# Kernel tuning notes

Measured on AMD Instinct MI355X. Metric: run time of the kernel, lower is better.

The kernel has to match this reference:

```python
import jax, jax.numpy as jnp
import numpy as np

ROWS, COLS, CH, K = 8, 8, 32, 3
D = ROWS * COLS * CH  # state_dim = 2048


def _conv1d(x, w, b):
    # x: (N, C_in, L), w: (C_out, C_in, K) -- SAME padding = kernel//2 for odd K
    out = jax.lax.conv_general_dilated(x, w, window_strides=(1,), padding='SAME',
                                       dimension_numbers=('NCH', 'OIH', 'NCH'))
    return out + b[None, :, None]


def _cell(x, h, c, wx, bx, wh, bh):
    # RowSharedConvLSTMCell: x (B,ROWS,C_in,COLS), h/c (B,ROWS,CH,COLS)
    B = x.shape[0]
    xr = x.reshape(B * ROWS, x.shape[2], COLS)
    hr = h.reshape(B * ROWS, CH, COLS)
    gates = _conv1d(xr, wx, bx) + _conv1d(hr, wh, bh)
    i, f, o, g = jnp.split(gates, 4, axis=1)
    cr = jax.nn.sigmoid(f) * c.reshape(B * ROWS, CH, COLS) + jax.nn.sigmoid(i) * jnp.tanh(g)
    hr2 = jax.nn.sigmoid(o) * jnp.tanh(cr)
    return hr2.reshape(B, ROWS, CH, COLS), cr.reshape(B, ROWS, CH, COLS)


def _inter(state, enc, w, b):
    # scores h_d^T H_e -> softmax over encoder positions -> context -> tanh fuse
    scores = jnp.einsum('bsd,bd->bs', enc, state)
    a = jax.nn.softmax(scores, axis=1)
    ctx = jnp.einsum('bsd,bs->bd', enc, a)
    return jnp.tanh(jnp.concatenate([state, ctx], axis=-1) @ w + b)


def _self_step(state, pre_hist, ref_hist, t, w, b):
    # score against refined history, aggregate pre-self history; causal mask i < t
    T = pre_hist.shape[0]
    scores = jnp.einsum('tbd,bd->bt', ref_hist, state)
    mask = (jnp.arange(T) < t)[None, :]
    a = jax.nn.softmax(jnp.where(mask, scores, -1e9), axis=1)
    ctx = jnp.einsum('tbd,bt->bd', pre_hist, a) * (t > 0)  # zero context at step 0
    return jnp.tanh(jnp.concatenate([state, ctx], axis=-1) @ w + b)


def _forward(x_flat, encoder_outputs, h0, c0,
             cx_w0, cx_b0, ch_w0, ch_b0, cx_w1, cx_b1, ch_w1, ch_b1,
             ia_w0, ia_b0, sa_w0, sa_b0, ia_w1, ia_b1, sa_w1, sa_b1,
             hw1, hb1, hw2, hb2, hw3, hb3):
    B, T, _ = x_flat.shape
    xseq = x_flat.reshape(B, T, ROWS, COLS)[:, :, :, None, :]   # (B,T,ROWS,1,COLS)
    xseq = jnp.transpose(xseq, (1, 0, 2, 3, 4))                 # (T,B,ROWS,1,COLS)
    zhist = jnp.zeros((T, B, D), x_flat.dtype)
    carry = (h0[0], c0[0], h0[1], c0[1], zhist, zhist, zhist, zhist)

    def step(carry, xs):
        hA, cA, hB, cB, p0, r0, p1, r1 = carry
        xt, t = xs
        # layer 0: ConvLSTM -> inter-attn -> self-attn
        hraw0, cn0 = _cell(xt, hA, cA, cx_w0, cx_b0, ch_w0, ch_b0)
        hi0 = _inter(hraw0.reshape(B, D), encoder_outputs, ia_w0, ia_b0)
        hr0 = _self_step(hi0, p0, r0, t, sa_w0, sa_b0)
        p0 = p0.at[t].set(hi0)
        r0 = r0.at[t].set(hr0)
        # layer 1, fed with refined layer-0 output reshaped to frame
        hraw1, cn1 = _cell(hr0.reshape(B, ROWS, CH, COLS), hB, cB, cx_w1, cx_b1, ch_w1, ch_b1)
        hi1 = _inter(hraw1.reshape(B, D), encoder_outputs, ia_w1, ia_b1)
        hr1 = _self_step(hi1, p1, r1, t, sa_w1, sa_b1)
        p1 = p1.at[t].set(hi1)
        r1 = r1.at[t].set(hr1)
        # prediction head (eval-mode dropout = identity)
        z = jax.nn.relu(hr1 @ hw1 + hb1)
        z = jax.nn.relu(z @ hw2 + hb2)
        logits = z @ hw3 + hb3
        # hidden carries raw ConvLSTM h (matches original new_hidden.append((h_raw, c_new)))
        return (hraw0, cn0, hraw1, cn1, p0, r0, p1, r1), logits

    _, logits_seq = jax.lax.scan(step, carry, (xseq, jnp.arange(T)))
    return jnp.transpose(logits_seq, (1, 0, 2))  # (B, T, output_dim)


def setup_inputs() -> dict:
    key = jax.random.key(0)
    ks = jax.random.split(key, 16)
    B, T, S, OUT = 128, 64, 128, 2
    n = jax.random.normal
    f32 = jnp.float32
    inp = {
        'x_flat': n(ks[0], (B, T, ROWS * COLS), f32),
        'encoder_outputs': n(ks[1], (B, S, D), f32) * 0.05,
        'h0': jnp.zeros((2, B, ROWS, CH, COLS), f32),
        'c0': jnp.zeros((2, B, ROWS, CH, COLS), f32),
        'cx_w0': n(ks[2], (4 * CH, 1, K), f32) / float(np.sqrt(1 * K)),
        'cx_b0': jnp.zeros((4 * CH,), f32),
        'ch_w0': n(ks[3], (4 * CH, CH, K), f32) / float(np.sqrt(CH * K)),
        'ch_b0': jnp.zeros((4 * CH,), f32),
        'cx_w1': n(ks[4], (4 * CH, CH, K), f32) / float(np.sqrt(CH * K)),
        'cx_b1': jnp.zeros((4 * CH,), f32),
        'ch_w1': n(ks[5], (4 * CH, CH, K), f32) / float(np.sqrt(CH * K)),
        'ch_b1': jnp.zeros((4 * CH,), f32),
        'ia_w0': n(ks[6], (2 * D, D), f32) / float(np.sqrt(2 * D)),
        'ia_b0': jnp.zeros((D,), f32),
        'sa_w0': n(ks[7], (2 * D, D), f32) / float(np.sqrt(2 * D)),
        'sa_b0': jnp.zeros((D,), f32),
        'ia_w1': n(ks[8], (2 * D, D), f32) / float(np.sqrt(2 * D)),
        'ia_b1': jnp.zeros((D,), f32),
        'sa_w1': n(ks[9], (2 * D, D), f32) / float(np.sqrt(2 * D)),
        'sa_b1': jnp.zeros((D,), f32),
        'hw1': n(ks[10], (D, 200), f32) / float(np.sqrt(D)),
        'hb1': jnp.zeros((200,), f32),
        'hw2': n(ks[11], (200, 50), f32) / float(np.sqrt(200.0)),
        'hb2': jnp.zeros((50,), f32),
        'hw3': n(ks[12], (50, OUT), f32) / float(np.sqrt(50.0)),
        'hb3': jnp.zeros((OUT,), f32),
    }
    return inp


def reference(x_flat, encoder_outputs, h0, c0,
              cx_w0, cx_b0, ch_w0, ch_b0, cx_w1, cx_b1, ch_w1, ch_b1,
              ia_w0, ia_b0, sa_w0, sa_b0, ia_w1, ia_b1, sa_w1, sa_b1,
              hw1, hb1, hw2, hb2, hw3, hb3):
    return _forward(x_flat, encoder_outputs, h0, c0,
                    cx_w0, cx_b0, ch_w0, ch_b0, cx_w1, cx_b1, ch_w1, ch_b1,
                    ia_w0, ia_b0, sa_w0, sa_b0, ia_w1, ia_b1, sa_w1, sa_b1,
                    hw1, hb1, hw2, hb2, hw3, hb3)
```

## Files before the change

### kernel.cpp

```cpp
#include <hip/hip_runtime.h>
#include <math.h>


typedef _Float16 f16;
typedef _Float16 f16x8 __attribute__((ext_vector_type(8)));
typedef _Float16 f16x4 __attribute__((ext_vector_type(4)));
typedef _Float16 f16x2 __attribute__((ext_vector_type(2)));
typedef float  f32x16 __attribute__((ext_vector_type(16)));
typedef float  f32x4v __attribute__((ext_vector_type(4)));
typedef float  f32x2v __attribute__((ext_vector_type(2)));
typedef unsigned short u16x8 __attribute__((ext_vector_type(8)));
typedef unsigned short u16x4 __attribute__((ext_vector_type(4)));

#define BD 262144
#define XGT 1048576

__device__ __forceinline__ unsigned short f2bf(float x){
  unsigned int u = __builtin_bit_cast(unsigned int, x);
  u += 0x7fffu + ((u >> 16) & 1u);
  return (unsigned short)(u >> 16);
}
__device__ __forceinline__ float bf2f(unsigned short h){
  unsigned int u = ((unsigned int)h) << 16;
  return __builtin_bit_cast(float, u);
}
__device__ __forceinline__ float sigmoidf_(float x){
  return 1.0f / (1.0f + __expf(-x));
}
__device__ __forceinline__ void g2l16(const void* g, void* l){
  __builtin_amdgcn_global_load_lds(
      (const __attribute__((address_space(1))) unsigned int*)g,
      (__attribute__((address_space(3))) unsigned int*)l,
      16, 0, 0);
}

__global__ __launch_bounds__(256) void k_transpose_f16(
    const float* __restrict__ src, f16* __restrict__ dhi,
    const int K, const int N)
{
  __shared__ float tile[32][33];
  const int n0 = blockIdx.x * 32, k0 = blockIdx.y * 32;
  const int tx = threadIdx.x & 31, ty = threadIdx.x >> 5;
  #pragma unroll
  for (int ii = 0; ii < 4; ++ii){
    const int k = k0 + ty + ii*8, n = n0 + tx;
    float v = (n < N) ? src[(size_t)k * N + n] : 0.0f;
    tile[ty + ii*8][tx] = v;
  }
  __syncthreads();
  #pragma unroll
  for (int ii = 0; ii < 4; ++ii){
    const int n = n0 + ty + ii*8, k = k0 + tx;
    dhi[(size_t)n * K + k] = (f16)tile[tx][ty + ii*8];
  }
}

__global__ __launch_bounds__(256) void k_enc_prep(
    const float* __restrict__ enc,
    f16* __restrict__ encF, f16* __restrict__ encT)
{
  __shared__ float tile[32][33];
  const int dt = blockIdx.x;
  const int st = blockIdx.y;
  const int b  = blockIdx.z;
  const int tx = threadIdx.x & 31, ty = threadIdx.x >> 5;
  const int d0 = dt*32, s0 = st*32;
  #pragma unroll
  for (int ii = 0; ii < 4; ++ii){
    const int s = s0 + ty + ii*8, d = d0 + tx;
    const float v = enc[((size_t)b*128 + s)*2048 + d];
    tile[ty + ii*8][tx] = v;
    encF[((size_t)b*128 + s)*2048 + d] = (f16)v;
  }
  __syncthreads();
  #pragma unroll
  for (int ii = 0; ii < 4; ++ii){
    const int d = d0 + ty + ii*8, s = s0 + tx;
    encT[((size_t)b*2048 + d)*128 + s] = (f16)tile[tx][ty + ii*8];
  }
}

__global__ void k_pack_cellw(const float* __restrict__ chw,
                             const float* __restrict__ cxw,
                             unsigned short* __restrict__ wh16,
                             unsigned short* __restrict__ wcx16)
{
  const int i = blockIdx.x * 256 + threadIdx.x;
  if (i < 128 * 32){
    const int gc = i >> 5, icg = i & 31;
    #pragma unroll
    for (int k = 0; k < 3; ++k){
      wh16[(icg*3 + k)*128 + gc]  = f2bf(chw[i*3 + k]);
      wcx16[(icg*3 + k)*128 + gc] = f2bf(cxw[i*3 + k]);
    }
  }
}

__global__ __launch_bounds__(256) void k_cell0(
    const float* __restrict__ x_flat,
    const float* __restrict__ h0, const float* __restrict__ c0,
    const float* __restrict__ cxw, const float* __restrict__ cxb,
    const float* __restrict__ chw, const float* __restrict__ chb,
    f16* __restrict__ hrawHi)
{
  const int b = blockIdx.x >> 3, row = blockIdx.x & 7;
  const int tid = threadIdx.x;
  __shared__ float h_lds[264];
  __shared__ float x_lds[8];
  __shared__ float P[128][2][9];
  const int gc = tid >> 1, ih = tid & 1;
  float wh[16][3];
  #pragma unroll
  for (int icl = 0; icl < 16; ++icl)
    #pragma unroll
    for (int k = 0; k < 3; ++k)
      wh[icl][k] = chw[(gc*32 + ih*16 + icl)*3 + k];
  const float wx0 = cxw[gc*3+0], wx1 = cxw[gc*3+1], wx2 = cxw[gc*3+2];
  const float bsum = cxb[gc] + chb[gc];
  const int ic = tid >> 3, col = tid & 7;
  const size_t dg = (size_t)b*2048 + row*256 + tid;
  const int wofs = tid + ((tid >> 7) << 2);
  const int hbase = ih * 132;
  float c_reg = c0[dg];
  h_lds[wofs] = h0[dg];
  float xnext = (tid < 8) ? x_flat[((size_t)b*64 + 0)*64 + row*8 + tid] : 0.f;
  __syncthreads();
  for (int t = 0; t < 64; ++t){
    if (tid < 8) x_lds[tid] = xnext;
    __syncthreads();
    if (t < 63 && tid < 8)
      xnext = x_flat[((size_t)b*64 + t + 1)*64 + row*8 + tid];
    float g8[8];
    #pragma unroll
    for (int c2 = 0; c2 < 8; ++c2) g8[c2] = 0.f;
    #pragma unroll
    for (int icl = 0; icl < 16; ++icl){
      const float* hb = &h_lds[icl*8 + hbase];
      f32x4v hv0 = *reinterpret_cast<const f32x4v*>(hb);
      f32x4v hv1 = *reinterpret_cast<const f32x4v*>(hb + 4);
      const float hv[8] = {hv0[0],hv0[1],hv0[2],hv0[3],hv1[0],hv1[1],hv1[2],hv1[3]};
      #pragma unroll
      for (int c2 = 0; c2 < 8; ++c2){
        float s = hv[c2] * wh[icl][1];
        if (c2 > 0) s += hv[c2-1] * wh[icl][0];
        if (c2 < 7) s += hv[c2+1] * wh[icl][2];
        g8[c2] += s;
      }
    }
    if (ih == 0){
      #pragma unroll
      for (int c2 = 0; c2 < 8; ++c2){
        float s = x_lds[c2] * wx1 + bsum;
        if (c2 > 0) s += x_lds[c2-1] * wx0;
        if (c2 < 7) s += x_lds[c2+1] * wx2;
        g8[c2] += s;
      }
    }
    #pragma unroll
    for (int c2 = 0; c2 < 8; ++c2) P[gc][ih][c2] = g8[c2];
    __syncthreads();
    const float ipre = P[ic   ][0][col] + P[ic   ][1][col];
    const float fpre = P[ic+32][0][col] + P[ic+32][1][col];
    const float opre = P[ic+64][0][col] + P[ic+64][1][col];
    const float gpre = P[ic+96][0][col] + P[ic+96][1][col];
    const float cn = sigmoidf_(fpre)*c_reg + sigmoidf_(ipre)*tanhf(gpre);
    c_reg = cn;
    const float hn = sigmoidf_(opre)*tanhf(cn);
    hrawHi[((size_t)t*128 + b)*2048 + row*256 + tid] = (f16)hn;
    __syncthreads();
    h_lds[wofs] = hn;
  }
}

__global__ __launch_bounds__(256) void k_xconv(
    const f16* __restrict__ r0Hi, const f16* __restrict__ r0Lo,
    const unsigned short* __restrict__ wcx16,
    f16* __restrict__ xg)
{
  const int b = blockIdx.x >> 3, row = blockIdx.x & 7;
  const int tc = blockIdx.y;
  const int tid = threadIdx.x;
  const int gc = tid >> 1, half = tid & 1;
  __shared__ float xs[8][256];
  __shared__ unsigned short wl[96*128];
  for (int i = tid; i < 96*128; i += 256) wl[i] = wcx16[i];
  const size_t dg = (size_t)b*2048 + row*256 + tid;
  #pragma unroll
  for (int tt = 0; tt < 8; ++tt){
    const size_t tb = (size_t)(tc*8 + tt)*BD + dg;
    xs[tt][tid] = (float)r0Hi[tb] + (float)r0Lo[tb];
  }
  __syncthreads();
  const int c0 = half*4;
  float acc0[8], acc1[8], acc2[8], acc3[8];
  #pragma unroll
  for (int tt = 0; tt < 8; ++tt){ acc0[tt]=0.f; acc1[tt]=0.f; acc2[tt]=0.f; acc3[tt]=0.f; }
  for (int ic2 = 0; ic2 < 32; ++ic2){
    const unsigned short* wq = &wl[ic2*3*128 + gc];
    const float wx0 = bf2f(wq[0]), wx1 = bf2f(wq[128]), wx2 = bf2f(wq[256]);
    #pragma unroll
    for (int tt = 0; tt < 8; ++tt){
      const float* xr = &xs[tt][ic2*8];
      {
        const int c = c0 + 0;
        float s = xr[c]*wx1;
        if (c > 0) s += xr[c-1]*wx0;
        s += xr[c+1]*wx2;
        acc0[tt] += s;
      }
      {
        const int c = c0 + 1;
        acc1[tt] += xr[c]*wx1 + xr[c-1]*wx0 + xr[c+1]*wx2;
      }
      {
        const int c = c0 + 2;
        acc2[tt] += xr[c]*wx1 + xr[c-1]*wx0 + xr[c+1]*wx2;
      }
      {
        const int c = c0 + 3;
        float s = xr[c]*wx1 + xr[c-1]*wx0;
        if (c < 7) s += xr[c+1]*wx2;
        acc3[tt] += s;
      }
    }
  }
  const size_t xgbase = ((size_t)b*8 + row)*1024 + gc*8 + half*4;
  #pragma unroll
  for (int tt = 0; tt < 8; ++tt){
    f16x4 o;
    o[0] = (f16)acc0[tt]; o[1] = (f16)acc1[tt];
    o[2] = (f16)acc2[tt]; o[3] = (f16)acc3[tt];
    *reinterpret_cast<f16x4*>(xg + (size_t)(tc*8 + tt)*XGT + xgbase) = o;
  }
}

__global__ __launch_bounds__(256) void k_cell1_all(
    const f16* __restrict__ xg,
    const float* __restrict__ h0s, const float* __restrict__ c0s,
    const unsigned short* __restrict__ wh16,
    const float* __restrict__ cxb, const float* __restrict__ chb,
    f16* __restrict__ hrw1Hi)
{
  const int b = blockIdx.x >> 3, row = blockIdx.x & 7;
  const int tid = threadIdx.x;
  __shared__ float h_lds[264];
  __shared__ float P[128][2][9];
  __shared__ unsigned short wlds16[96*128];
  const int gc = tid >> 1, ih = tid & 1;
  for (int i = tid; i < 96*128; i += 256) wlds16[i] = wh16[i];
  const size_t dg = (size_t)b*2048 + row*256 + tid;
  const int ic = tid >> 3, col = tid & 7;
  const float bi = cxb[ic]    + chb[ic];
  const float bf = cxb[ic+32] + chb[ic+32];
  const float bo = cxb[ic+64] + chb[ic+64];
  const float bg = cxb[ic+96] + chb[ic+96];
  const int wofs = tid + ((tid >> 7) << 2);
  const int hbase = ih * 132;
  const size_t xgbase = ((size_t)b*8 + row)*1024 + gc*8;
  float c_reg = c0s[dg];
  h_lds[wofs] = h0s[dg];
  f16x8 xgv;
  if (ih == 0) xgv = *reinterpret_cast<const f16x8*>(xg + xgbase);
  __syncthreads();
  for (int t = 0; t < 64; ++t){
    f16x8 xgn;
    if (ih == 0 && t < 63)
      xgn = *reinterpret_cast<const f16x8*>(xg + (size_t)(t+1)*XGT + xgbase);
    {
      float g8[8];
      #pragma unroll
      for (int c2 = 0; c2 < 8; ++c2) g8[c2] = 0.f;
      #pragma unroll
      for (int icl = 0; icl < 16; ++icl){
        const int icg = ih*16 + icl;
        const float* hb = &h_lds[icl*8 + hbase];
        f32x4v hv0 = *reinterpret_cast<const f32x4v*>(hb);
        f32x4v hv1 = *reinterpret_cast<const f32x4v*>(hb + 4);
        const float hv[8] = {hv0[0],hv0[1],hv0[2],hv0[3],hv1[0],hv1[1],hv1[2],hv1[3]};
        const unsigned short* wq = &wlds16[icg*3*128 + gc];
        const float wh0 = bf2f(wq[0]);
        const float wh1 = bf2f(wq[128]);
        const float wh2 = bf2f(wq[256]);
        #pragma unroll
        for (int c2 = 0; c2 < 8; ++c2){
          float s = hv[c2]*wh1;
          if (c2 > 0) s += hv[c2-1]*wh0;
          if (c2 < 7) s += hv[c2+1]*wh2;
          g8[c2] += s;
        }
      }
      if (ih == 0){
        #pragma unroll
        for (int c2 = 0; c2 < 8; ++c2) g8[c2] += (float)xgv[c2];
      }
      #pragma unroll
      for (int c2 = 0; c2 < 8; ++c2) P[gc][ih][c2] = g8[c2];
    }
    __syncthreads();
    {
      const float ipre = P[ic   ][0][col] + P[ic   ][1][col] + bi;
      const float fpre = P[ic+32][0][col] + P[ic+32][1][col] + bf;
      const float opre = P[ic+64][0][col] + P[ic+64][1][col] + bo;
      const float gpre = P[ic+96][0][col] + P[ic+96][1][col] + bg;
      const float cn = sigmoidf_(fpre)*c_reg + sigmoidf_(ipre)*tanhf(gpre);
      c_reg = cn;
      const float hraw = sigmoidf_(opre)*tanhf(cn);
      hrw1Hi[(size_t)t*BD + dg] = (f16)hraw;
      __syncthreads();
      h_lds[wofs] = hraw;
      if (ih == 0) xgv = xgn;
    }
  }
}

__global__ __launch_bounds__(256) void k_attn(
    const f16* __restrict__ encF,
    const f16* __restrict__ encT,
    const f16* __restrict__ stHi,
    f16* __restrict__ ctxHi)
{
  const int b = blockIdx.x, th = blockIdx.y;
  const int tid = threadIdx.x, lane = tid & 63, wv = tid >> 6;
  __shared__ float S_lds[128][36];
  __shared__ float red[8][32];
  __shared__ float colv[32];
  __shared__ __align__(16) char aT[8192];
  const int kb = lane >> 5;
  {
    const int rA = wv*32 + (lane & 31);
    const int tcol = th*32 + (lane & 31);
    const f16* pA  = encF + ((size_t)b*128 + rA)*2048 + kb*8;
    const f16* pBH = stHi + ((size_t)tcol*128 + b)*2048 + kb*8;
    f32x16 acc;
    #pragma unroll
    for (int r = 0; r < 16; ++r) acc[r] = 0.f;
    #pragma unroll 4
    for (int s = 0; s < 128; ++s){
      f16x8 av = *reinterpret_cast<const f16x8*>(pA  + s*16);
      f16x8 bh = *reinterpret_cast<const f16x8*>(pBH + s*16);
      acc = __builtin_amdgcn_mfma_f32_32x32x16_f16(av, bh, acc, 0, 0, 0);
    }
    #pragma unroll
    for (int r = 0; r < 16; ++r){
      const int rr = 4*kb + (r & 3) + 8*(r >> 2);
      S_lds[wv*32 + rr][lane & 31] = acc[r];
    }
  }
  __syncthreads();
  {
    const int c = tid & 31, g = tid >> 5;
    float ev[16];
    float m = -INFINITY;
    #pragma unroll
    for (int i = 0; i < 16; ++i){ ev[i] = S_lds[g*16 + i][c]; m = fmaxf(m, ev[i]); }
    red[g][c] = m;
    __syncthreads();
    if (tid < 32){
      float M = red[0][tid];
      #pragma unroll
      for (int j = 1; j < 8; ++j) M = fmaxf(M, red[j][tid]);
      colv[tid] = M;
    }
    __syncthreads();
    const float M = colv[c];
    float sum = 0.f;
    #pragma unroll
    for (int i = 0; i < 16; ++i){ ev[i] = __expf(ev[i] - M); sum += ev[i]; }
    __syncthreads();
    red[g][c] = sum;
    __syncthreads();
    if (tid < 32){
      float L = red[0][tid];
      #pragma unroll
      for (int j = 1; j < 8; ++j) L += red[j][tid];
      colv[tid] = 1.f / L;
    }
    __syncthreads();
    const float inv = colv[c];
    f16x8 w0, w1;
    #pragma unroll
    for (int j = 0; j < 8; ++j){
      w0[j] = (f16)(ev[j] * inv);
      w1[j] = (f16)(ev[8 + j] * inv);
    }
    const int sw = (c & 15) << 4;
    *reinterpret_cast<f16x8*>(aT + c*256 + (((g*2    )*16) ^ sw)) = w0;
    *reinterpret_cast<f16x8*>(aT + c*256 + (((g*2 + 1)*16) ^ sw)) = w1;
  }
  __syncthreads();
  {
    const int arow = lane & 31;
    const int asw = (arow & 15) << 4;
    f16x8 afr[8];
    #pragma unroll
    for (int ks = 0; ks < 8; ++ks){
      const int chunk = 2*ks + kb;
      afr[ks] = *reinterpret_cast<const f16x8*>(aT + arow*256 + ((chunk*16) ^ asw));
    }
    for (int nt = wv; nt < 64; nt += 4){
      const int d = nt*32 + (lane & 31);
      const f16* pB = encT + ((size_t)b*2048 + d)*128 + kb*8;
      f32x16 acc;
      #pragma unroll
      for (int r = 0; r < 16; ++r) acc[r] = 0.f;
      #pragma unroll
      for (int ks = 0; ks < 8; ++ks){
        f16x8 bv = *reinterpret_cast<const f16x8*>(pB + ks*16);
        acc = __builtin_amdgcn_mfma_f32_32x32x16_f16(afr[ks], bv, acc, 0, 0, 0);
      }
      #pragma unroll
      for (int r = 0; r < 16; ++r){
        const int rr = 4*kb + (r & 3) + 8*(r >> 2);
        const size_t o = ((size_t)(th*32 + rr)*128 + b)*2048 + d;
        ctxHi[o] = (f16)acc[r];
      }
    }
  }
}

__global__ __launch_bounds__(256, 2) void k_gemm_full(
    const f16* __restrict__ a0, const f16* __restrict__ a1,
    const f16* __restrict__ wHp, const float* __restrict__ bias,
    f16* __restrict__ outHi, f16* __restrict__ outLo)
{
  const int nt = blockIdx.x, t = blockIdx.y;
  const size_t tb = (size_t)t * BD;
  const int tid = threadIdx.x;
  const int lane = tid & 63, wv = tid >> 6;
  __shared__ __align__(16) char lds[49152];
  const f16* wH = wHp + (size_t)(nt*64)*4096;

  auto stage = [&](int buf, int ki){
    char* lb = lds + buf*24576;
    const f16* aH = ((ki < 32) ? a0 : a1) + tb;
    const int ke = (ki & 31) * 64;
    #pragma unroll
    for (int i = 0; i < 4; ++i){
      const int c = i*256 + tid, row = c >> 3;
      const int srcb = ((c & 7)*16) ^ ((row & 7) << 4);
      g2l16((const char*)(aH + (size_t)row*2048 + ke) + srcb, lb + c*16);
    }
    #pragma unroll
    for (int i = 0; i < 2; ++i){
      const int c = i*256 + tid, row = c >> 3;
      const int srcb = ((c & 7)*16) ^ ((row & 7) << 4);
      g2l16((const char*)(wH + (size_t)row*4096 + ki*64) + srcb, lb + 16384 + c*16);
    }
  };

  f32x16 acc0, acc1;
  #pragma unroll
  for (int r = 0; r < 16; ++r){ acc0[r] = 0.f; acc1[r] = 0.f; }
  const int rA = wv*32 + (lane & 31);
  const int kb = lane >> 5;
  const int rB0 = lane & 31;
  const int aswz = (rA & 7) << 4;
  const int bswz = (rB0 & 7) << 4;

  stage(0, 0);
  __syncthreads();
  for (int ki = 0; ki < 64; ++ki){
    const int buf = ki & 1;
    if (ki < 63) stage(buf ^ 1, ki + 1);
    const char* lb = lds + buf*24576;
    #pragma unroll
    for (int s = 0; s < 4; ++s){
      const int cb = s*32 + kb*16;
      f16x8 ah  = *reinterpret_cast<const f16x8*>(lb + rA*128 + (cb ^ aswz));
      f16x8 b0h = *reinterpret_cast<const f16x8*>(lb + 16384 + rB0*128 + (cb ^ bswz));
      f16x8 b1h = *reinterpret_cast<const f16x8*>(lb + 16384 + 4096 + rB0*128 + (cb ^ bswz));
      acc0 = __builtin_amdgcn_mfma_f32_32x32x16_f16(ah, b0h, acc0, 0, 0, 0);
      acc1 = __builtin_amdgcn_mfma_f32_32x32x16_f16(ah, b1h, acc1, 0, 0, 0);
    }
    __syncthreads();
  }

  const int col0 = nt*64 + (lane & 31);
  const float b0 = bias[col0], b1 = bias[col0 + 32];
  const int rowBase = wv*32 + 4*kb;
  #pragma unroll
  for (int r = 0; r < 16; ++r){
    const int rr = rowBase + (r & 3) + 8*(r >> 2);
    const size_t o = tb + (size_t)rr*2048 + col0;
    const float p = tanhf(acc0[r] + b0);
    const float q = tanhf(acc1[r] + b1);
    const f16 ph = (f16)p, qh = (f16)q;
    outHi[o]      = ph;  outLo[o]      = (f16)(p - (float)ph);
    outHi[o + 32] = qh;  outLo[o + 32] = (f16)(q - (float)qh);
  }
}

__global__ __launch_bounds__(256, 2) void k_gemm_full2(
    const f16* __restrict__ aHi,
    const f16* __restrict__ wSp,
    float* __restrict__ Y, f16* __restrict__ G)
{
  const int nt = blockIdx.x, t = blockIdx.y;
  const size_t tb = (size_t)t * BD;
  const int tid = threadIdx.x;
  const int lane = tid & 63, wv = tid >> 6;
  __shared__ __align__(16) char lds[49152];
  const f16* wH = wSp + (size_t)(nt*64)*2048;
  const f16* aH = aHi + tb;

  auto stage = [&](int buf, int ki){
    char* lb = lds + buf*24576;
    const int ke = ki*64;
    #pragma unroll
    for (int i = 0; i < 4; ++i){
      const int c = i*256 + tid, row = c >> 3;
      const int srcb = ((c & 7)*16) ^ ((row & 7) << 4);
      g2l16((const char*)(aH + (size_t)row*2048 + ke) + srcb, lb + c*16);
    }
    #pragma unroll
    for (int i = 0; i < 2; ++i){
      const int c = i*256 + tid, row = c >> 3;
      const int srcb = ((c & 7)*16) ^ ((row & 7) << 4);
      g2l16((const char*)(wH + (size_t)row*2048 + ke) + srcb, lb + 16384 + c*16);
    }
  };

  f32x16 acc0, acc1;
  #pragma unroll
  for (int r = 0; r < 16; ++r){ acc0[r] = 0.f; acc1[r] = 0.f; }
  const int rA = wv*32 + (lane & 31);
  const int kb = lane >> 5;
  const int rB0 = lane & 31;
  const int aswz = (rA & 7) << 4;
  const int bswz = (rB0 & 7) << 4;

  stage(0, 0);
  __syncthreads();
  for (int ki = 0; ki < 32; ++ki){
    const int buf = ki & 1;
    if (ki < 31) stage(buf ^ 1, ki + 1);
    const char* lb = lds + buf*24576;
    #pragma unroll
    for (int s = 0; s < 4; ++s){
      const int cb = s*32 + kb*16;
      f16x8 ah  = *reinterpret_cast<const f16x8*>(lb + rA*128 + (cb ^ aswz));
      f16x8 b0h = *reinterpret_cast<const f16x8*>(lb + 16384 + rB0*128 + (cb ^ bswz));
      f16x8 b1h = *reinterpret_cast<const f16x8*>(lb + 16384 + 4096 + rB0*128 + (cb ^ bswz));
      acc0 = __builtin_amdgcn_mfma_f32_32x32x16_f16(ah, b0h, acc0, 0, 0, 0);
      acc1 = __builtin_amdgcn_mfma_f32_32x32x16_f16(ah, b1h, acc1, 0, 0, 0);
    }
    __syncthreads();
  }

  const int col0 = nt*64 + (lane & 31);
  const int rowBase = wv*32 + 4*kb;
  if (nt < 32){
    float* yp = Y + tb + col0;
    #pragma unroll
    for (int r = 0; r < 16; ++r){
      const int rr = rowBase + (r & 3) + 8*(r >> 2);
      yp[(size_t)rr*2048]      = acc0[r];
      yp[(size_t)rr*2048 + 32] = acc1[r];
    }
  } else {
    f16* gp = G + tb + (col0 - 2048);
    #pragma unroll
    for (int r = 0; r < 16; ++r){
      const int rr = rowBase + (r & 3) + 8*(r >> 2);
      gp[(size_t)rr*2048]      = (f16)acc0[r];
      gp[(size_t)rr*2048 + 32] = (f16)acc1[r];
    }
  }
}

__global__ __launch_bounds__(1024) void k_selfchain(
    const f16* __restrict__ pHi, const f16* __restrict__ pLo,
    const float* __restrict__ Y, const f16* __restrict__ G,
    const float* __restrict__ bias,
    f16* __restrict__ rHi, f16* __restrict__ rLo)
{
  const int b = blockIdx.x;
  const int tid = threadIdx.x, lane = tid & 63, wv = tid >> 6;
  __shared__ float sc[64];
  __shared__ float a_lds[64];
  const int d0 = tid * 2;
  f32x2v bb = *reinterpret_cast<const f32x2v*>(bias + d0);
  for (int t = 0; t < 64; ++t){
    const size_t pb = ((size_t)t*128 + b)*2048;
    if (t > 0){
      float hreg[32];
      #pragma unroll
      for (int jj = 0; jj < 4; ++jj){
        const int d = (jj*64 + lane)*8;
        f16x8 h8 = *reinterpret_cast<const f16x8*>(pHi + pb + d);
        f16x8 l8 = *reinterpret_cast<const f16x8*>(pLo + pb + d);
        #pragma unroll
        for (int j = 0; j < 8; ++j) hreg[jj*8+j] = (float)h8[j] + (float)l8[j];
      }
      for (int i = wv; i < t; i += 16){
        const f16* rh = rHi + ((size_t)i*128 + b)*2048;
        const f16* rl = rLo + ((size_t)i*128 + b)*2048;
        float dot = 0.f;
        #pragma unroll
        for (int jj = 0; jj < 4; ++jj){
          const int d = (jj*64 + lane)*8;
          f16x8 h8 = *reinterpret_cast<const f16x8*>(rh + d);
          f16x8 l8 = *reinterpret_cast<const f16x8*>(rl + d);
          #pragma unroll
          for (int j = 0; j < 8; ++j)
            dot += ((float)h8[j] + (float)l8[j]) * hreg[jj*8+j];
        }
        #pragma unroll
        for (int off = 1; off < 64; off <<= 1) dot += __shfl_xor(dot, off);
        if (lane == 0) sc[i] = dot;
      }
      __syncthreads();
      if (tid < 64){
        const float s = (tid < t) ? sc[tid] : -INFINITY;
        float mm = s;
        #pragma unroll
        for (int off = 1; off < 64; off <<= 1) mm = fmaxf(mm, __shfl_xor(mm, off));
        const float e = (tid < t) ? __expf(s - mm) : 0.f;
        float sum = e;
        #pragma unroll
        for (int off = 1; off < 64; off <<= 1) sum += __shfl_xor(sum, off);
        a_lds[tid] = e / sum;
      }
      __syncthreads();
    }
    float y0, y1;
    {
      f32x2v yv = *reinterpret_cast<const f32x2v*>(Y + (size_t)t*BD + (size_t)b*2048 + d0);
      y0 = yv[0] + bb[0];
      y1 = yv[1] + bb[1];
    }
    if (t > 0){
      float z0 = 0.f, z1 = 0.f;
      int i = 0;
      for (; i + 1 < t; i += 2){
        const float a0 = a_lds[i], a1 = a_lds[i+1];
        f16x2 g0 = *reinterpret_cast<const f16x2*>(G + ((size_t)i*128 + b)*2048 + d0);
        f16x2 g1 = *reinterpret_cast<const f16x2*>(G + ((size_t)(i+1)*128 + b)*2048 + d0);
        y0 += a0 * (float)g0[0];
        y1 += a0 * (float)g0[1];
        z0 += a1 * (float)g1[0];
        z1 += a1 * (float)g1[1];
      }
      if (i < t){
        const float a0 = a_lds[i];
        f16x2 g0 = *reinterpret_cast<const f16x2*>(G + ((size_t)i*128 + b)*2048 + d0);
        y0 += a0 * (float)g0[0];
        y1 += a0 * (float)g0[1];
      }
      y0 += z0;
      y1 += z1;
    }
    f16x2 hh, ll;
    {
      const float v0 = tanhf(y0);
      const float v1 = tanhf(y1);
      hh[0] = (f16)v0; ll[0] = (f16)(v0 - (float)hh[0]);
      hh[1] = (f16)v1; ll[1] = (f16)(v1 - (float)hh[1]);
    }
    *reinterpret_cast<f16x2*>(rHi + pb + d0) = hh;
    *reinterpret_cast<f16x2*>(rLo + pb + d0) = ll;
    __syncthreads();
  }
}

__global__ __launch_bounds__(256) void k_headgemm(
    const f16* __restrict__ aHi,
    const f16* __restrict__ w1H,
    const float* __restrict__ hb1,
    float* __restrict__ z1)
{
  const int mb = blockIdx.x;
  const int nt = blockIdx.y;
  const int lane = threadIdx.x & 63, wv = threadIdx.x >> 6;
  const int rowA = mb*128 + wv*32 + (lane & 31);
  const int kb = lane >> 5;
  const int n = nt*32 + (lane & 31);
  const f16* pAH = aHi + (size_t)rowA*2048 + kb*8;
  const f16* pBH = w1H + (size_t)n*2048 + kb*8;
  f32x16 acc;
  #pragma unroll
  for (int r = 0; r < 16; ++r) acc[r] = 0.f;
  #pragma unroll 4
  for (int s = 0; s < 128; ++s){
    f16x8 ah = *reinterpret_cast<const f16x8*>(pAH + s*16);
    f16x8 bh = *reinterpret_cast<const f16x8*>(pBH + s*16);
    acc = __builtin_amdgcn_mfma_f32_32x32x16_f16(ah, bh, acc, 0, 0, 0);
  }
  const float bias = (n < 200) ? hb1[n] : 0.f;
  const int rowBase = mb*128 + wv*32 + 4*kb;
  #pragma unroll
  for (int r = 0; r < 16; ++r){
    const int rr = rowBase + (r & 3) + 8*(r >> 2);
    z1[(size_t)rr*224 + n] = fmaxf(acc[r] + bias, 0.f);
  }
}

__global__ __launch_bounds__(256) void k_head2(
    const float* __restrict__ z1,
    const float* __restrict__ hw2, const float* __restrict__ hb2,
    const float* __restrict__ hw3, const float* __restrict__ hb3,
    float* __restrict__ out)
{
  const int r0 = blockIdx.x * 64;
  const int tid = threadIdx.x;
  __shared__ float zl[64][200];
  __shared__ float z2[64][50];
  for (int i = tid; i < 64*200; i += 256){
    const int r = i / 200, n = i % 200;
    zl[r][n] = z1[(size_t)(r0 + r)*224 + n];
  }
  __syncthreads();
  for (int i = tid; i < 64*50; i += 256){
    const int r = i / 50, n = i % 50;
    float s = hb2[n];
    for (int k = 0; k < 200; ++k) s += zl[r][k] * hw2[k*50 + n];
    z2[r][n] = fmaxf(s, 0.f);
  }
  __syncthreads();
  for (int i = tid; i < 128; i += 256){
    const int r = i >> 1, c = i & 1;
    float s = hb3[c];
    for (int k = 0; k < 50; ++k) s += z2[r][k] * hw3[k*2 + c];
    const int rg = r0 + r;
    const int tt = rg >> 7, b = rg & 127;
    out[(size_t)b*128 + tt*2 + c] = s;
  }
}

extern "C" void kernel_launch(void* const* d_in, const int* in_sizes, int n_in,
                              void* d_out, int out_size, void* d_ws, size_t ws_size,
                              hipStream_t stream)
{
  (void)in_sizes; (void)n_in; (void)out_size; (void)ws_size;
  const float* x_flat = (const float*)d_in[0];
  const float* enc    = (const float*)d_in[1];
  const float* h0     = (const float*)d_in[2];
  const float* c0     = (const float*)d_in[3];
  const float* cx_w0  = (const float*)d_in[4];
  const float* cx_b0  = (const float*)d_in[5];
  const float* ch_w0  = (const float*)d_in[6];
  const float* ch_b0  = (const float*)d_in[7];
  const float* cx_w1  = (const float*)d_in[8];
  const float* cx_b1  = (const float*)d_in[9];
  const float* ch_w1  = (const float*)d_in[10];
  const float* ch_b1  = (const float*)d_in[11];
  const float* ia_w0  = (const float*)d_in[12];
  const float* ia_b0  = (const float*)d_in[13];
  const float* sa_w0  = (const float*)d_in[14];
  const float* sa_b0  = (const float*)d_in[15];
  const float* ia_w1  = (const float*)d_in[16];
  const float* ia_b1  = (const float*)d_in[17];
  const float* sa_w1  = (const float*)d_in[18];
  const float* sa_b1  = (const float*)d_in[19];
  const float* hw1    = (const float*)d_in[20];
  const float* hb1    = (const float*)d_in[21];
  const float* hw2    = (const float*)d_in[22];
  const float* hb2    = (const float*)d_in[23];
  const float* hw3    = (const float*)d_in[24];
  const float* hb3    = (const float*)d_in[25];
  float* out = (float*)d_out;

  char* ws = (char*)d_ws;
  size_t off = 0;
  auto alloc = [&](size_t bytes) -> char* {
    char* p = ws + off;
    off += (bytes + 255) & ~(size_t)255;
    return p;
  };
  const size_t WPLANE = (size_t)2048*4096*2;
  const size_t TPLANE = (size_t)64*BD*2;
  f16* wIa0 = (f16*)alloc(WPLANE);
  f16* wSa0 = (f16*)alloc(WPLANE);
  f16* wIa1 = (f16*)alloc(WPLANE);
  f16* wSa1 = (f16*)alloc(WPLANE);
  f16* w1H  = (f16*)alloc((size_t)224*2048*2);
  f16* encF = (f16*)alloc((size_t)128*128*2048*2);
  f16* encT = (f16*)alloc((size_t)128*2048*128*2);
  f16* S1 = (f16*)alloc(TPLANE);
  f16* S2 = (f16*)alloc(TPLANE);
  f16* S3 = (f16*)alloc(TPLANE);
  f16* S4 = (f16*)alloc(TPLANE);
  f16* S5 = (f16*)alloc(TPLANE);
  f16* S6 = (f16*)alloc(TPLANE);
  f16* S7 = (f16*)alloc(TPLANE);
  f16* S8 = (f16*)alloc(TPLANE);
  unsigned short* wh16  = (unsigned short*)alloc((size_t)96*128*2);
  unsigned short* wcx16 = (unsigned short*)alloc((size_t)96*128*2);
  f16*  hr0AHi = S1;
  f16*  ctx0Hi = S3;
  f16*  p0Hi   = S5;  f16* p0Lo   = S6;
  float* Y0 = (float*)S1;
  f16*  G0  = S3;
  f16*  r0Hi = S7;    f16* r0Lo   = S8;
  f16*  xgb  = S1;
  f16*  hrw1Hi = S5;
  f16*  ctx1Hi = S1;
  f16*  p1Hi = S7;    f16* p1Lo   = S8;
  float* Y1 = (float*)S1;
  f16*  G1  = S4;
  f16*  r1Hi = S5;    f16* r1Lo   = S3;
  float* z1 = (float*)wSa0;

  k_transpose_f16<<<dim3(64,128),256,0,stream>>>(ia_w0, wIa0, 4096, 2048);
  k_transpose_f16<<<dim3(64,128),256,0,stream>>>(ia_w1, wIa1, 4096, 2048);
  k_transpose_f16<<<dim3(64,64),256,0,stream>>>(sa_w0, wSa0, 2048, 2048);
  k_transpose_f16<<<dim3(64,64),256,0,stream>>>(sa_w0 + (size_t)2048*2048,
                                                wSa0 + (size_t)2048*2048, 2048, 2048);
  k_transpose_f16<<<dim3(64,64),256,0,stream>>>(sa_w1, wSa1, 2048, 2048);
  k_transpose_f16<<<dim3(64,64),256,0,stream>>>(sa_w1 + (size_t)2048*2048,
                                                wSa1 + (size_t)2048*2048, 2048, 2048);
  k_transpose_f16<<<dim3(7,64),256,0,stream>>>(hw1, w1H, 2048, 200);
  k_enc_prep<<<dim3(64,4,128),256,0,stream>>>(enc, encF, encT);
  k_pack_cellw<<<16,256,0,stream>>>(ch_w1, cx_w1, wh16, wcx16);

  k_cell0<<<1024,256,0,stream>>>(x_flat, h0, c0, cx_w0, cx_b0, ch_w0, ch_b0,
                                 hr0AHi);
  k_attn<<<dim3(128,2),256,0,stream>>>(encF, encT, hr0AHi, ctx0Hi);
  k_gemm_full<<<dim3(32,64),256,0,stream>>>(hr0AHi, ctx0Hi,
                                            wIa0, ia_b0, p0Hi, p0Lo);
  k_gemm_full2<<<dim3(64,64),256,0,stream>>>(p0Hi, wSa0, Y0, G0);
  k_selfchain<<<128,1024,0,stream>>>(p0Hi, p0Lo, Y0, G0, sa_b0, r0Hi, r0Lo);

  k_xconv<<<dim3(1024,8),256,0,stream>>>(r0Hi, r0Lo, wcx16, xgb);
  k_cell1_all<<<1024,256,0,stream>>>(xgb,
                                     h0 + (size_t)128*2048, c0 + (size_t)128*2048,
                                     wh16, cx_b1, ch_b1, hrw1Hi);
  k_attn<<<dim3(128,2),256,0,stream>>>(encF, encT, hrw1Hi, ctx1Hi);
  k_gemm_full<<<dim3(32,64),256,0,stream>>>(hrw1Hi, ctx1Hi,
                                            wIa1, ia_b1, p1Hi, p1Lo);
  k_gemm_full2<<<dim3(64,64),256,0,stream>>>(p1Hi, wSa1, Y1, G1);
  k_selfchain<<<128,1024,0,stream>>>(p1Hi, p1Lo, Y1, G1, sa_b1, r1Hi, r1Lo);

  k_headgemm<<<dim3(64,7),256,0,stream>>>(r1Hi, w1H, hb1, z1);
  k_head2<<<128,256,0,stream>>>(z1, hw2, hb2, hw3, hb3, out);
}
```

Baseline: 3.585 ms.

## Split self-attention chain into 16-step chunks with batched cross-chunk score kernel

The sequential self-attention chain now runs as four chunked launches of 16 steps each. Scores against refined states from finished chunks are computed ahead of time by a separate parallel kernel into a score matrix, using refined rows held in LDS. Inside a chunk only the intra-chunk dot products stay on the serial path, one per wave. This shortens the per-step serial work and spreads the cross-chunk score work over more blocks, at the cost of extra launches and a score-matrix buffer.

```diff
diff --git a/kernel.cpp b/kernel.cpp
--- a/kernel.cpp
+++ b/kernel.cpp
@@ -568,11 +568,76 @@
   }
 }
 
-__global__ __launch_bounds__(1024) void k_selfchain(
+__global__ __launch_bounds__(512) void k_scores(
+    const f16* __restrict__ rHi, const f16* __restrict__ rLo,
+    const f16* __restrict__ pHi, const f16* __restrict__ pLo,
+    float* __restrict__ Smat,
+    const int i0)
+{
+  const int b = blockIdx.x, ih = blockIdx.y;
+  const int tid = threadIdx.x, lane = tid & 63, wv = tid >> 6;
+  const int ibase = i0 + 8*ih;
+  __shared__ float rs[8*2112];
+  {
+    const int row = tid >> 6;
+    const int d0 = lane * 32;
+    const f16* rh = rHi + ((size_t)(ibase + row)*128 + b)*2048 + d0;
+    const f16* rl = rLo + ((size_t)(ibase + row)*128 + b)*2048 + d0;
+    #pragma unroll
+    for (int q = 0; q < 4; ++q){
+      f16x8 h8 = *reinterpret_cast<const f16x8*>(rh + q*8);
+      f16x8 l8 = *reinterpret_cast<const f16x8*>(rl + q*8);
+      #pragma unroll
+      for (int j = 0; j < 8; ++j){
+        const int d = d0 + q*8 + j;
+        rs[row*2112 + d + (d >> 5)] = (float)h8[j] + (float)l8[j];
+      }
+    }
+  }
+  __syncthreads();
+  for (int tp = i0 + 16 + wv; tp < 64; tp += 8){
+    const int d0 = lane * 32;
+    const f16* ph = pHi + ((size_t)tp*128 + b)*2048 + d0;
+    const f16* pl = pLo + ((size_t)tp*128 + b)*2048 + d0;
+    float pv[32];
+    #pragma unroll
+    for (int q = 0; q < 4; ++q){
+      f16x8 h8 = *reinterpret_cast<const f16x8*>(ph + q*8);
+      f16x8 l8 = *reinterpret_cast<const f16x8*>(pl + q*8);
+      #pragma unroll
+      for (int j = 0; j < 8; ++j) pv[q*8+j] = (float)h8[j] + (float)l8[j];
+    }
+    float dots[8];
+    #pragma unroll
+    for (int i = 0; i < 8; ++i){
+      const float* rr = &rs[i*2112 + lane*33];
+      float acc = 0.f;
+      #pragma unroll
+      for (int j = 0; j < 32; ++j) acc += rr[j] * pv[j];
+      dots[i] = acc;
+    }
+    #pragma unroll
+    for (int i = 0; i < 8; ++i){
+      float v = dots[i];
+      #pragma unroll
+      for (int off = 1; off < 64; off <<= 1) v += __shfl_xor(v, off);
+      dots[i] = v;
+    }
+    if (lane == 0){
+      float* so = Smat + ((size_t)b*64 + tp)*64 + ibase;
+      #pragma unroll
+      for (int i = 0; i < 8; ++i) so[i] = dots[i];
+    }
+  }
+}
+
+__global__ __launch_bounds__(1024) void k_selfchain_c(
     const f16* __restrict__ pHi, const f16* __restrict__ pLo,
     const float* __restrict__ Y, const f16* __restrict__ G,
     const float* __restrict__ bias,
-    f16* __restrict__ rHi, f16* __restrict__ rLo)
+    f16* __restrict__ rHi, f16* __restrict__ rLo,
+    const float* __restrict__ Smat,
+    const int t0)
 {
   const int b = blockIdx.x;
   const int tid = threadIdx.x, lane = tid & 63, wv = tid >> 6;
@@ -580,19 +645,21 @@
   __shared__ float a_lds[64];
   const int d0 = tid * 2;
   f32x2v bb = *reinterpret_cast<const f32x2v*>(bias + d0);
-  for (int t = 0; t < 64; ++t){
+  for (int t = t0; t < t0 + 16; ++t){
     const size_t pb = ((size_t)t*128 + b)*2048;
     if (t > 0){
-      float hreg[32];
-      #pragma unroll
-      for (int jj = 0; jj < 4; ++jj){
-        const int d = (jj*64 + lane)*8;
-        f16x8 h8 = *reinterpret_cast<const f16x8*>(pHi + pb + d);
-        f16x8 l8 = *reinterpret_cast<const f16x8*>(pLo + pb + d);
+      if (tid < t0) sc[tid] = Smat[((size_t)b*64 + t)*64 + tid];
+      if (wv < t - t0){
+        float hreg[32];
         #pragma unroll
-        for (int j = 0; j < 8; ++j) hreg[jj*8+j] = (float)h8[j] + (float)l8[j];
-      }
-      for (int i = wv; i < t; i += 16){
+        for (int jj = 0; jj < 4; ++jj){
+          const int d = (jj*64 + lane)*8;
+          f16x8 h8 = *reinterpret_cast<const f16x8*>(pHi + pb + d);
+          f16x8 l8 = *reinterpret_cast<const f16x8*>(pLo + pb + d);
+          #pragma unroll
+          for (int j = 0; j < 8; ++j) hreg[jj*8+j] = (float)h8[j] + (float)l8[j];
+        }
+        const int i = t0 + wv;
         const f16* rh = rHi + ((size_t)i*128 + b)*2048;
         const f16* rl = rLo + ((size_t)i*128 + b)*2048;
         float dot = 0.f;
@@ -786,6 +853,7 @@
   f16* S8 = (f16*)alloc(TPLANE);
   unsigned short* wh16  = (unsigned short*)alloc((size_t)96*128*2);
   unsigned short* wcx16 = (unsigned short*)alloc((size_t)96*128*2);
+  float* Smat = (float*)alloc((size_t)128*64*64*4);
   f16*  hr0AHi = S1;
   f16*  ctx0Hi = S3;
   f16*  p0Hi   = S5;  f16* p0Lo   = S6;
@@ -819,7 +887,12 @@
   k_gemm_full<<<dim3(32,64),256,0,stream>>>(hr0AHi, ctx0Hi,
                                             wIa0, ia_b0, p0Hi, p0Lo);
   k_gemm_full2<<<dim3(64,64),256,0,stream>>>(p0Hi, wSa0, Y0, G0);
-  k_selfchain<<<128,1024,0,stream>>>(p0Hi, p0Lo, Y0, G0, sa_b0, r0Hi, r0Lo);
+  for (int c = 0; c < 4; ++c){
+    k_selfchain_c<<<128,1024,0,stream>>>(p0Hi, p0Lo, Y0, G0, sa_b0,
+                                         r0Hi, r0Lo, Smat, c*16);
+    if (c < 3)
+      k_scores<<<dim3(128,2),512,0,stream>>>(r0Hi, r0Lo, p0Hi, p0Lo, Smat, c*16);
+  }
 
   k_xconv<<<dim3(1024,8),256,0,stream>>>(r0Hi, r0Lo, wcx16, xgb);
   k_cell1_all<<<1024,256,0,stream>>>(xgb,
@@ -829,7 +902,12 @@
   k_gemm_full<<<dim3(32,64),256,0,stream>>>(hrw1Hi, ctx1Hi,
                                             wIa1, ia_b1, p1Hi, p1Lo);
   k_gemm_full2<<<dim3(64,64),256,0,stream>>>(p1Hi, wSa1, Y1, G1);
-  k_selfchain<<<128,1024,0,stream>>>(p1Hi, p1Lo, Y1, G1, sa_b1, r1Hi, r1Lo);
+  for (int c = 0; c < 4; ++c){
+    k_selfchain_c<<<128,1024,0,stream>>>(p1Hi, p1Lo, Y1, G1, sa_b1,
+                                         r1Hi, r1Lo, Smat, c*16);
+    if (c < 3)
+      k_scores<<<dim3(128,2),512,0,stream>>>(r1Hi, r1Lo, p1Hi, p1Lo, Smat, c*16);
+  }
 
   k_headgemm<<<dim3(64,7),256,0,stream>>>(r1Hi, w1H, hb1, z1);
   k_head2<<<128,256,0,stream>>>(z1, hw2, hb2, hw3, hb3, out);
```

Measured after the change: 3.815 ms. 6.4% more time.
